# Kernel tuning notes

Hardware: AMD Instinct MI355X
Metric: run time of the kernel (lower is better)

## Reference

```python
import jax, jax.numpy as jnp
import numpy as np

N, D, DFF, E, TOPK = 32768, 256, 1024, 8, 2


def setup_inputs() -> dict:
    key = jax.random.key(0)
    ks = jax.random.split(key, 5)
    return {
        "x": jax.random.normal(ks[0], (N, D), dtype=jnp.float32),
        "gate_w": jax.random.normal(ks[1], (D, E), dtype=jnp.float32) * 0.02,
        "gate_b": jnp.zeros((E,), jnp.float32),
        "w1": jax.random.normal(ks[2], (E, D, DFF), dtype=jnp.float32) * 0.02,
        "b1": jnp.zeros((E, DFF), jnp.float32),
        "w2": jax.random.normal(ks[3], (E, DFF, D), dtype=jnp.float32) * 0.02,
        "b2": jnp.zeros((E, D), jnp.float32),
        "top_k": TOPK,
    }


def reference(x, gate_w, gate_b, w1, b1, w2, b2, top_k):
    # Gating network: linear -> softmax -> top-k (returns topk_vals, topk_idx)
    logits = x @ gate_w + gate_b                       # [N, E]
    probs = jax.nn.softmax(logits, axis=-1)
    topk_vals, topk_idx = jax.lax.top_k(probs, top_k)  # [N, K], [N, K]

    # Naive full-batch expert evaluation (every expert runs on every token),
    # faithful to the original loop that applies the selected expert to all of x.
    h = jax.nn.relu(jnp.einsum('nd,edf->enf', x, w1) + b1[:, None, :])  # [E, N, DFF]
    y = jnp.einsum('enf,efd->end', h, w2) + b2[:, None, :]              # [E, N, D]

    # Per-token gather of the top-k experts' outputs, then weighted sum.
    y = jnp.transpose(y, (1, 0, 2))                                      # [N, E, D]
    sel = jnp.take_along_axis(y, topk_idx[:, :, None], axis=1)           # [N, K, D]
    return jnp.sum(sel * topk_vals[:, :, None], axis=1)                  # [N, D]
```

## Files before the change

kernel.cpp:

```cpp
#include <hip/hip_runtime.h>

#define N_TOK 32768
#define D 256
#define DFF 1024
#define NE 8
#define TB 64

typedef __attribute__((ext_vector_type(16))) float f32x16;
typedef __attribute__((ext_vector_type(8)))  short bf16x8;

#define BARRIER() do {                                        \
    asm volatile("s_waitcnt lgkmcnt(0)" ::: "memory");        \
    __builtin_amdgcn_s_barrier();                             \
    __builtin_amdgcn_sched_barrier(0);                        \
} while (0)

__device__ __forceinline__ unsigned cvtpk(float lo, float hi) {
    unsigned r;
    asm("v_cvt_pk_bf16_f32 %0, %1, %2" : "=v"(r) : "v"(lo), "v"(hi));
    return r;
}

__global__ __launch_bounds__(256) void prep_gate(
    const float* __restrict__ w1, const float* __restrict__ w2,
    short* __restrict__ w1f, short* __restrict__ w2f,
    const float* __restrict__ x, short* __restrict__ xb,
    const float* __restrict__ gw, const float* __restrict__ gb,
    int* __restrict__ cnt, int* __restrict__ bidx, float* __restrict__ bp,
    int2* __restrict__ opos) {
    const int b = blockIdx.x;
    if (b >= 128) {
        if (b < 1152) {
            const int gid  = (b - 128) * 256 + threadIdx.x;
            const int lane = gid & 63;
            const int frag = gid >> 6;
            const int dblk = frag & 15;
            const int fblk = (frag >> 4) & 31;
            const int e    = frag >> 9;
            const int l31 = lane & 31, g = lane >> 5;

            const float* src = w1 + ((size_t)e * 256 + dblk * 16 + g * 8) * 1024
                                  + fblk * 32 + l31;
            unsigned u[4];
#pragma unroll
            for (int jp = 0; jp < 4; ++jp)
                u[jp] = cvtpk(src[(size_t)(jp * 2) * 1024],
                              src[(size_t)(jp * 2 + 1) * 1024]);
            *(uint4*)(w1f + (size_t)gid * 8) = make_uint4(u[0], u[1], u[2], u[3]);
        } else {
            const int gid  = (b - 1152) * 256 + threadIdx.x;
            const int lane = gid & 63;
            const int frag = gid >> 6;
            const int fblk = frag & 63;
            const int cblk = (frag >> 6) & 7;
            const int e    = frag >> 9;
            const int l31 = lane & 31, g = lane >> 5;

            const float* src = w2 + ((size_t)e * 1024 + fblk * 16 + g * 8) * 256
                                  + cblk * 32 + l31;
            unsigned u[4];
#pragma unroll
            for (int jp = 0; jp < 4; ++jp)
                u[jp] = cvtpk(src[(size_t)(jp * 2) * 256],
                              src[(size_t)(jp * 2 + 1) * 256]);
            *(uint4*)(w2f + (size_t)gid * 8) = make_uint4(u[0], u[1], u[2], u[3]);
        }
        return;
    }

    __shared__ float gws[2048];
    __shared__ int   se1[256], se2[256];
    __shared__ float sp1[256], sp2[256];
    __shared__ int   hist[NE], base_[NE];

    const int tid = threadIdx.x;
#pragma unroll
    for (int i = 0; i < 8; ++i) gws[tid + 256 * i] = gw[tid + 256 * i];
    if (tid < NE) hist[tid] = 0;
    __syncthreads();

    const int t = b * 256 + tid;
    const float* xr = x + (size_t)t * D;
    short* xbr = xb + (size_t)t * D;

    double acc[NE];
#pragma unroll
    for (int e = 0; e < NE; ++e) acc[e] = 0.0;

    for (int d0 = 0; d0 < 256; d0 += 8) {
        float4 xv0 = *(const float4*)(xr + d0);
        float4 xv1 = *(const float4*)(xr + d0 + 4);
        float xa[8] = {xv0.x, xv0.y, xv0.z, xv0.w, xv1.x, xv1.y, xv1.z, xv1.w};
#pragma unroll
        for (int j = 0; j < 8; ++j) {
            float4 ga  = *(const float4*)&gws[(d0 + j) * 8];
            float4 gbb = *(const float4*)&gws[(d0 + j) * 8 + 4];
            double xd = (double)xa[j];
            acc[0] += xd * (double)ga.x;  acc[1] += xd * (double)ga.y;
            acc[2] += xd * (double)ga.z;  acc[3] += xd * (double)ga.w;
            acc[4] += xd * (double)gbb.x; acc[5] += xd * (double)gbb.y;
            acc[6] += xd * (double)gbb.z; acc[7] += xd * (double)gbb.w;
        }
        uint4 o;
        o.x = cvtpk(xv0.x, xv0.y);  o.y = cvtpk(xv0.z, xv0.w);
        o.z = cvtpk(xv1.x, xv1.y);  o.w = cvtpk(xv1.z, xv1.w);
        *(uint4*)(xbr + d0) = o;
    }

    double l[NE];
#pragma unroll
    for (int e = 0; e < NE; ++e) l[e] = acc[e] + (double)gb[e];
    int e1 = 0;
#pragma unroll
    for (int e = 1; e < NE; ++e) if (l[e] > l[e1]) e1 = e;
    int e2 = (e1 == 0) ? 1 : 0;
#pragma unroll
    for (int e = 0; e < NE; ++e) if (e != e1 && l[e] > l[e2]) e2 = e;

    double s = 0.0;
#pragma unroll
    for (int e = 0; e < NE; ++e) s += exp(l[e] - l[e1]);
    se1[tid] = e1; se2[tid] = e2;
    sp1[tid] = (float)(1.0 / s);
    sp2[tid] = (float)(exp(l[e2] - l[e1]) / s);
    __syncthreads();

    const int pos1 = atomicAdd(&hist[se1[tid]], 1);
    const int pos2 = atomicAdd(&hist[se2[tid]], 1);
    __syncthreads();
    if (tid < NE) base_[tid] = atomicAdd(&cnt[tid], hist[tid]);
    __syncthreads();

    const int o1 = se1[tid] * N_TOK + base_[se1[tid]] + pos1;
    const int o2 = se2[tid] * N_TOK + base_[se2[tid]] + pos2;
    bidx[o1] = t;  bp[o1] = sp1[tid];
    bidx[o2] = t;  bp[o2] = sp2[tid];
    opos[t] = make_int2(o1, o2);
}

__global__ __launch_bounds__(512, 4) void expert_ffn(
    const short* __restrict__ xb,
    const short* __restrict__ w1f,
    const short* __restrict__ w2f,
    const float* __restrict__ b1, const float* __restrict__ b2,
    const int* __restrict__ cnt, const int* __restrict__ bidx,
    const float* __restrict__ bp, float* __restrict__ out,
    float* __restrict__ yp, int staged) {
    const int e    = blockIdx.x & 7;
    const int tile = blockIdx.x >> 3;
    const int n_e  = cnt[e];
    const int row0 = tile * TB;
    if (row0 >= n_e) return;

    __shared__ short xs[16 * 64 * 16];
    __shared__ short hs[32 * 512];
    __shared__ int   tok_s[TB];
    __shared__ float p_s[TB];

    const int tid  = threadIdx.x;
    const int lane = tid & 63, wid = tid >> 6;
    const int l31  = lane & 31, g = lane >> 5;

    int cbase = 0;
    for (int j = 0; j < e; ++j) cbase += cnt[j];

    if (tid < TB) {
        int r = row0 + tid;
        tok_s[tid] = (r < n_e) ? bidx[e * N_TOK + r] : -1;
        p_s[tid]   = (r < n_e) ? bp[e * N_TOK + r] : 0.f;
    }
    BARRIER();

    {
        const int tok = tid >> 3;
        const int tk  = tok_s[tok];
        const short* xrow = xb + (size_t)(tk < 0 ? 0 : tk) * D;
#pragma unroll
        for (int i = 0; i < 2; ++i) {
            const int dblk = (tid & 7) * 2 + i;
            uint4 v0 = make_uint4(0, 0, 0, 0), v1 = make_uint4(0, 0, 0, 0);
            if (tk >= 0) {
                v0 = *(const uint4*)(xrow + dblk * 16);
                v1 = *(const uint4*)(xrow + dblk * 16 + 8);
            }
            short* dp = &xs[dblk * 1024 + tok * 16];
            *(uint4*)(dp)     = v0;
            *(uint4*)(dp + 8) = v1;
        }
    }

    f32x16 acc[2];
#pragma unroll
    for (int a = 0; a < 2; ++a)
#pragma unroll
        for (int r = 0; r < 16; ++r) acc[a][r] = 0.f;

    const short* w1e = w1f + (size_t)e * (32 * 16 * 512);
    const short* w2e = w2f + (size_t)e * (8 * 64 * 512);
    const float* b1e = b1 + e * DFF;

    BARRIER();

    for (int fc = 0; fc < 4; ++fc) {
        f32x16 h0, h1;
#pragma unroll
        for (int r = 0; r < 16; ++r) { h0[r] = 0.f; h1[r] = 0.f; }

        const short* w1p = w1e + ((size_t)(fc * 8 + wid) * 16) * 512 + lane * 8;
        __builtin_amdgcn_s_setprio(1);
        {
            bf16x8 a0 = *(const bf16x8*)(w1p);
            bf16x8 x0 = *(const bf16x8*)&xs[l31 * 16 + g * 8];
            bf16x8 x1 = *(const bf16x8*)&xs[512 + l31 * 16 + g * 8];
#pragma unroll
            for (int db = 0; db < 16; ++db) {
                bf16x8 an, y0, y1;
                if (db < 15) {
                    an = *(const bf16x8*)(w1p + (db + 1) * 512);
                    y0 = *(const bf16x8*)&xs[(db + 1) * 1024 + l31 * 16 + g * 8];
                    y1 = *(const bf16x8*)&xs[(db + 1) * 1024 + 512 + l31 * 16 + g * 8];
                }
                h0 = __builtin_amdgcn_mfma_f32_32x32x16_bf16(a0, x0, h0, 0, 0, 0);
                h1 = __builtin_amdgcn_mfma_f32_32x32x16_bf16(a0, x1, h1, 0, 0, 0);
                if (db < 15) { a0 = an; x0 = y0; x1 = y1; }
            }
        }
        __builtin_amdgcn_s_setprio(0);

        BARRIER();

#pragma unroll
        for (int tp = 0; tp < 2; ++tp) {
            const f32x16& hh = tp ? h1 : h0;
#pragma unroll
            for (int m = 0; m < 4; ++m) {
                float4 bq = *(const float4*)(b1e + fc * 256 + wid * 32 + 8 * m + 4 * g);
                float v0 = fmaxf(hh[4 * m + 0] + bq.x, 0.f);
                float v1 = fmaxf(hh[4 * m + 1] + bq.y, 0.f);
                float v2 = fmaxf(hh[4 * m + 2] + bq.z, 0.f);
                float v3 = fmaxf(hh[4 * m + 3] + bq.w, 0.f);
                uint2 pk;
                pk.x = cvtpk(v0, v1);
                pk.y = cvtpk(v2, v3);
                const int fragid = (2 * wid + (m >> 1)) * 2 + tp;
                *(uint2*)&hs[fragid * 512 + ((m & 1) * 32 + l31) * 8 + 4 * g] = pk;
            }
        }

        const short* w2p = w2e + ((size_t)wid * 64 + fc * 16) * 512 + lane * 8;
        bf16x8 wcur = *(const bf16x8*)(w2p);

        BARRIER();

        __builtin_amdgcn_s_setprio(1);
        {
            bf16x8 ha0 = *(const bf16x8*)&hs[0 * 512 + lane * 8];
            bf16x8 ha1 = *(const bf16x8*)&hs[1 * 512 + lane * 8];
#pragma unroll
            for (int kt = 0; kt < 16; ++kt) {
                bf16x8 wn, hb0, hb1;
                if (kt < 15) {
                    wn  = *(const bf16x8*)(w2p + (kt + 1) * 512);
                    hb0 = *(const bf16x8*)&hs[((kt + 1) * 2 + 0) * 512 + lane * 8];
                    hb1 = *(const bf16x8*)&hs[((kt + 1) * 2 + 1) * 512 + lane * 8];
                }
                acc[0] = __builtin_amdgcn_mfma_f32_32x32x16_bf16(ha0, wcur, acc[0], 0, 0, 0);
                acc[1] = __builtin_amdgcn_mfma_f32_32x32x16_bf16(ha1, wcur, acc[1], 0, 0, 0);
                if (kt < 15) { wcur = wn; ha0 = hb0; ha1 = hb1; }
            }
        }
        __builtin_amdgcn_s_setprio(0);
    }

    const float* b2e = b2 + e * D;
    const int col = wid * 32 + l31;
    const float bv = b2e[col];
    if (staged) {
        float* ype = yp + ((size_t)(cbase + row0)) * 256;
#pragma unroll
        for (int tp = 0; tp < 2; ++tp) {
#pragma unroll
            for (int r = 0; r < 16; ++r) {
                const int tl = tp * 32 + (r & 3) + 8 * (r >> 2) + 4 * g;
                if (tok_s[tl] >= 0)
                    __builtin_nontemporal_store(
                        (acc[tp][r] + bv) * p_s[tl],
                        &ype[(size_t)tl * 256 + col]);
            }
        }
    } else {
#pragma unroll
        for (int tp = 0; tp < 2; ++tp) {
#pragma unroll
            for (int r = 0; r < 16; ++r) {
                const int tl = tp * 32 + (r & 3) + 8 * (r >> 2) + 4 * g;
                const int tk = tok_s[tl];
                if (tk >= 0)
                    atomicAdd(out + (size_t)tk * D + col,
                              (acc[tp][r] + bv) * p_s[tl]);
            }
        }
    }
}

__global__ __launch_bounds__(256) void combine(
    const float* __restrict__ yp, const int2* __restrict__ opos,
    const int* __restrict__ cnt, float* __restrict__ out) {
    __shared__ int cb[NE];
    if (threadIdx.x == 0) {
        int s = 0;
#pragma unroll
        for (int j = 0; j < NE; ++j) { cb[j] = s; s += cnt[j]; }
    }
    __syncthreads();
    const int gid   = blockIdx.x * 256 + threadIdx.x;
    const int t     = gid >> 6;
    const int lane4 = gid & 63;
    const int2 o = opos[t];
    const size_t r1 = (size_t)(cb[o.x >> 15] + (o.x & (N_TOK - 1)));
    const size_t r2 = (size_t)(cb[o.y >> 15] + (o.y & (N_TOK - 1)));
    const float4 a = ((const float4*)yp)[r1 * 64 + lane4];
    const float4 b = ((const float4*)yp)[r2 * 64 + lane4];
    float4 r;
    r.x = a.x + b.x; r.y = a.y + b.y; r.z = a.z + b.z; r.w = a.w + b.w;
    ((float4*)out)[gid] = r;
}

extern "C" void kernel_launch(void* const* d_in, const int* in_sizes, int n_in,
                              void* d_out, int out_size, void* d_ws, size_t ws_size,
                              hipStream_t stream) {
    const float* x  = (const float*)d_in[0];
    const float* gw = (const float*)d_in[1];
    const float* gb = (const float*)d_in[2];
    const float* w1 = (const float*)d_in[3];
    const float* b1 = (const float*)d_in[4];
    const float* w2 = (const float*)d_in[5];
    const float* b2 = (const float*)d_in[6];
    float* out = (float*)d_out;

    char* ws = (char*)d_ws;
    size_t off = 0;
    int*   cnt   = (int*)(ws + off);  off += 256;
    int*   bidx  = (int*)(ws + off);  off += (size_t)NE * N_TOK * 4;
    float* bp    = (float*)(ws + off); off += (size_t)NE * N_TOK * 4;
    int2*  opos  = (int2*)(ws + off); off += (size_t)N_TOK * 8;
    short* w1f   = (short*)(ws + off); off += (size_t)NE * D * DFF * 2;
    short* w2f   = (short*)(ws + off); off += (size_t)NE * D * DFF * 2;
    short* xb    = (short*)(ws + off); off += (size_t)N_TOK * D * 2;
    float* yp    = (float*)(ws + off); off += (size_t)2 * N_TOK * D * 4;
    const int staged = (ws_size >= off) ? 1 : 0;

    hipMemsetAsync(cnt, 0, 256, stream);
    if (!staged)
        hipMemsetAsync(d_out, 0, (size_t)out_size * sizeof(float), stream);

    prep_gate<<<128 + 2048, 256, 0, stream>>>(
        w1, w2, w1f, w2f, x, xb, gw, gb, cnt, bidx, bp, opos);
    expert_ffn<<<NE * (N_TOK / TB), 512, 0, stream>>>(xb, w1f, w2f, b1, b2,
                                                      cnt, bidx, bp, out, yp, staged);
    if (staged)
        combine<<<(N_TOK * D / 4) / 256, 256, 0, stream>>>(yp, opos, cnt, out);
}
```

Before: 145.2 us.

## Software-pipeline expert FFN chunks by interleaving next GEMM1 with current GEMM2

Restructures the per-chunk loop so that the first-layer GEMM for chunk fc+1 runs in the same unrolled loop as the second-layer GEMM for chunk fc. The two MFMA streams and their global and LDS loads interleave, hiding load latency and the barrier and pack stall between stages. The barrier count per iteration stays the same, but the change holds more live registers (extra accumulators g0/g1 and extra operand prefetches), which may raise register pressure or reduce occupancy.

```diff
diff --git a/kernel.cpp b/kernel.cpp
--- a/kernel.cpp
+++ b/kernel.cpp
@@ -201,12 +201,34 @@
 
     BARRIER();
 
-    for (int fc = 0; fc < 4; ++fc) {
+#define PACK(FC, H0, H1)                                                      \
+    do {                                                                      \
+        _Pragma("unroll")                                                     \
+        for (int tp = 0; tp < 2; ++tp) {                                      \
+            const f32x16& hh = tp ? (H1) : (H0);                              \
+            _Pragma("unroll")                                                 \
+            for (int m = 0; m < 4; ++m) {                                     \
+                float4 bq = *(const float4*)(b1e + (FC) * 256 + wid * 32 +    \
+                                             8 * m + 4 * g);                  \
+                float v0 = fmaxf(hh[4 * m + 0] + bq.x, 0.f);                  \
+                float v1 = fmaxf(hh[4 * m + 1] + bq.y, 0.f);                  \
+                float v2 = fmaxf(hh[4 * m + 2] + bq.z, 0.f);                  \
+                float v3 = fmaxf(hh[4 * m + 3] + bq.w, 0.f);                  \
+                uint2 pk;                                                     \
+                pk.x = cvtpk(v0, v1);                                         \
+                pk.y = cvtpk(v2, v3);                                         \
+                const int fragid = (2 * wid + (m >> 1)) * 2 + tp;             \
+                *(uint2*)&hs[fragid * 512 + ((m & 1) * 32 + l31) * 8 + 4 * g] \
+                    = pk;                                                     \
+            }                                                                 \
+        }                                                                     \
+    } while (0)
+
+    {
         f32x16 h0, h1;
 #pragma unroll
         for (int r = 0; r < 16; ++r) { h0[r] = 0.f; h1[r] = 0.f; }
-
-        const short* w1p = w1e + ((size_t)(fc * 8 + wid) * 16) * 512 + lane * 8;
+        const short* w1p = w1e + ((size_t)(0 * 8 + wid) * 16) * 512 + lane * 8;
         __builtin_amdgcn_s_setprio(1);
         {
             bf16x8 a0 = *(const bf16x8*)(w1p);
@@ -226,51 +248,72 @@
             }
         }
         __builtin_amdgcn_s_setprio(0);
-
-        BARRIER();
-
-#pragma unroll
-        for (int tp = 0; tp < 2; ++tp) {
-            const f32x16& hh = tp ? h1 : h0;
-#pragma unroll
-            for (int m = 0; m < 4; ++m) {
-                float4 bq = *(const float4*)(b1e + fc * 256 + wid * 32 + 8 * m + 4 * g);
-                float v0 = fmaxf(hh[4 * m + 0] + bq.x, 0.f);
-                float v1 = fmaxf(hh[4 * m + 1] + bq.y, 0.f);
-                float v2 = fmaxf(hh[4 * m + 2] + bq.z, 0.f);
-                float v3 = fmaxf(hh[4 * m + 3] + bq.w, 0.f);
-                uint2 pk;
-                pk.x = cvtpk(v0, v1);
-                pk.y = cvtpk(v2, v3);
-                const int fragid = (2 * wid + (m >> 1)) * 2 + tp;
-                *(uint2*)&hs[fragid * 512 + ((m & 1) * 32 + l31) * 8 + 4 * g] = pk;
-            }
-        }
-
+        PACK(0, h0, h1);
+    }
+    BARRIER();
+
+    for (int fc = 0; fc < 4; ++fc) {
         const short* w2p = w2e + ((size_t)wid * 64 + fc * 16) * 512 + lane * 8;
-        bf16x8 wcur = *(const bf16x8*)(w2p);
-
-        BARRIER();
-
-        __builtin_amdgcn_s_setprio(1);
-        {
-            bf16x8 ha0 = *(const bf16x8*)&hs[0 * 512 + lane * 8];
-            bf16x8 ha1 = *(const bf16x8*)&hs[1 * 512 + lane * 8];
-#pragma unroll
-            for (int kt = 0; kt < 16; ++kt) {
-                bf16x8 wn, hb0, hb1;
-                if (kt < 15) {
-                    wn  = *(const bf16x8*)(w2p + (kt + 1) * 512);
-                    hb0 = *(const bf16x8*)&hs[((kt + 1) * 2 + 0) * 512 + lane * 8];
-                    hb1 = *(const bf16x8*)&hs[((kt + 1) * 2 + 1) * 512 + lane * 8];
+        if (fc < 3) {
+            const short* w1p = w1e + ((size_t)((fc + 1) * 8 + wid) * 16) * 512 + lane * 8;
+            f32x16 g0, g1;
+#pragma unroll
+            for (int r = 0; r < 16; ++r) { g0[r] = 0.f; g1[r] = 0.f; }
+
+            __builtin_amdgcn_s_setprio(1);
+            {
+                bf16x8 wcur = *(const bf16x8*)(w2p);
+                bf16x8 ha0  = *(const bf16x8*)&hs[0 * 512 + lane * 8];
+                bf16x8 ha1  = *(const bf16x8*)&hs[1 * 512 + lane * 8];
+                bf16x8 a0   = *(const bf16x8*)(w1p);
+                bf16x8 x0   = *(const bf16x8*)&xs[l31 * 16 + g * 8];
+                bf16x8 x1   = *(const bf16x8*)&xs[512 + l31 * 16 + g * 8];
+#pragma unroll
+                for (int s = 0; s < 16; ++s) {
+                    bf16x8 wn, hb0, hb1, an, y0, y1;
+                    if (s < 15) {
+                        wn  = *(const bf16x8*)(w2p + (s + 1) * 512);
+                        hb0 = *(const bf16x8*)&hs[((s + 1) * 2 + 0) * 512 + lane * 8];
+                        hb1 = *(const bf16x8*)&hs[((s + 1) * 2 + 1) * 512 + lane * 8];
+                        an  = *(const bf16x8*)(w1p + (s + 1) * 512);
+                        y0  = *(const bf16x8*)&xs[(s + 1) * 1024 + l31 * 16 + g * 8];
+                        y1  = *(const bf16x8*)&xs[(s + 1) * 1024 + 512 + l31 * 16 + g * 8];
+                    }
+                    acc[0] = __builtin_amdgcn_mfma_f32_32x32x16_bf16(ha0, wcur, acc[0], 0, 0, 0);
+                    acc[1] = __builtin_amdgcn_mfma_f32_32x32x16_bf16(ha1, wcur, acc[1], 0, 0, 0);
+                    g0 = __builtin_amdgcn_mfma_f32_32x32x16_bf16(a0, x0, g0, 0, 0, 0);
+                    g1 = __builtin_amdgcn_mfma_f32_32x32x16_bf16(a0, x1, g1, 0, 0, 0);
+                    if (s < 15) { wcur = wn; ha0 = hb0; ha1 = hb1; a0 = an; x0 = y0; x1 = y1; }
                 }
-                acc[0] = __builtin_amdgcn_mfma_f32_32x32x16_bf16(ha0, wcur, acc[0], 0, 0, 0);
-                acc[1] = __builtin_amdgcn_mfma_f32_32x32x16_bf16(ha1, wcur, acc[1], 0, 0, 0);
-                if (kt < 15) { wcur = wn; ha0 = hb0; ha1 = hb1; }
-            }
-        }
-        __builtin_amdgcn_s_setprio(0);
-    }
+            }
+            __builtin_amdgcn_s_setprio(0);
+
+            BARRIER();
+            PACK(fc + 1, g0, g1);
+            BARRIER();
+        } else {
+            __builtin_amdgcn_s_setprio(1);
+            {
+                bf16x8 wcur = *(const bf16x8*)(w2p);
+                bf16x8 ha0 = *(const bf16x8*)&hs[0 * 512 + lane * 8];
+                bf16x8 ha1 = *(const bf16x8*)&hs[1 * 512 + lane * 8];
+#pragma unroll
+                for (int kt = 0; kt < 16; ++kt) {
+                    bf16x8 wn, hb0, hb1;
+                    if (kt < 15) {
+                        wn  = *(const bf16x8*)(w2p + (kt + 1) * 512);
+                        hb0 = *(const bf16x8*)&hs[((kt + 1) * 2 + 0) * 512 + lane * 8];
+                        hb1 = *(const bf16x8*)&hs[((kt + 1) * 2 + 1) * 512 + lane * 8];
+                    }
+                    acc[0] = __builtin_amdgcn_mfma_f32_32x32x16_bf16(ha0, wcur, acc[0], 0, 0, 0);
+                    acc[1] = __builtin_amdgcn_mfma_f32_32x32x16_bf16(ha1, wcur, acc[1], 0, 0, 0);
+                    if (kt < 15) { wcur = wn; ha0 = hb0; ha1 = hb1; }
+                }
+            }
+            __builtin_amdgcn_s_setprio(0);
+        }
+    }
+#undef PACK
 
     const float* b2e = b2 + e * D;
     const int col = wid * 32 + l31;
```

Result: slower. 165.1 us (+13.7%).
